# Kernel optimization log

Hardware: AMD Instinct MI355X
Metric: run time of the kernel (lower is better)

## Reference

```python
import jax, jax.numpy as jnp
import numpy as np

NUM_ITER = 3
NUM_SLOTS = 8
SLOT_SIZE = 128
MLP_HIDDEN = 256
EPSILON = 1e-8
INPUT_SIZE = 128
LN_EPS = 1e-5


def layer_norm(x):
    # parameter-free LayerNorm over last dim (LayerNorm() built with no args)
    mu = jnp.mean(x, axis=-1, keepdims=True)
    var = jnp.mean(jnp.square(x - mu), axis=-1, keepdims=True)
    return (x - mu) * jax.lax.rsqrt(var + LN_EPS)


def setup_inputs() -> dict:
    key = jax.random.key(0)
    ks = jax.random.split(key, 16)
    B, N, Din, D, H = 128, 4096, INPUT_SIZE, SLOT_SIZE, MLP_HIDDEN
    s_in = 1.0 / np.sqrt(Din)
    s_d = 1.0 / np.sqrt(D)
    s_h = 1.0 / np.sqrt(H)
    return {
        "inputs": jax.random.normal(ks[0], (B, N, Din), jnp.float32),
        "slots_noise": jax.random.normal(ks[1], (B, NUM_SLOTS, D), jnp.float32),
        "slots_mu": jax.random.normal(ks[2], (1, 1, D), jnp.float32),
        "slots_log_sigma": jax.random.normal(ks[3], (1, 1, D), jnp.float32) * 0.1,
        "Wq": jax.random.normal(ks[4], (D, D), jnp.float32) * s_d,
        "Wk": jax.random.normal(ks[5], (D, Din), jnp.float32) * s_in,
        "Wv": jax.random.normal(ks[6], (D, Din), jnp.float32) * s_in,
        "W_ih": jax.random.normal(ks[7], (3 * D, D), jnp.float32) * s_d,
        "W_hh": jax.random.normal(ks[8], (3 * D, D), jnp.float32) * s_d,
        "b_ih": jax.random.normal(ks[9], (3 * D,), jnp.float32) * s_d,
        "b_hh": jax.random.normal(ks[10], (3 * D,), jnp.float32) * s_d,
        "W1": jax.random.normal(ks[11], (H, D), jnp.float32) * s_d,
        "b1": jnp.zeros((H,), jnp.float32),
        "W2": jax.random.normal(ks[12], (D, H), jnp.float32) * s_h,
        "b2": jnp.zeros((D,), jnp.float32),
    }


def gru_cell(x, h, W_ih, W_hh, b_ih, b_hh):
    # PyTorch GRU, single step. x, h: (..., D)
    gx = x @ W_ih.T + b_ih  # (..., 3D)
    gh = h @ W_hh.T + b_hh
    D = h.shape[-1]
    xr, xz, xn = gx[..., :D], gx[..., D:2 * D], gx[..., 2 * D:]
    hr, hz, hn = gh[..., :D], gh[..., D:2 * D], gh[..., 2 * D:]
    r = jax.nn.sigmoid(xr + hr)
    z = jax.nn.sigmoid(xz + hz)
    n = jnp.tanh(xn + r * hn)
    return (1.0 - z) * n + z * h


def reference(inputs, slots_noise, slots_mu, slots_log_sigma, Wq, Wk, Wv,
              W_ih, W_hh, b_ih, b_hh, W1, b1, W2, b2):
    scale = 1.0 / np.sqrt(SLOT_SIZE)
    x = layer_norm(inputs)                      # (B, N, Din)
    k = x @ Wk.T                                # (B, N, D)
    v = x @ Wv.T                                # (B, N, D)
    slots = slots_mu + jnp.exp(slots_log_sigma) * slots_noise  # (B, S, D)
    for _ in range(NUM_ITER):
        slots_n = layer_norm(slots)             # NOTE: GRU hidden is the NORMED slots (matches source)
        q = slots_n @ Wq.T                      # (B, S, D)
        logits = jnp.einsum("bnd,bsd->bns", k, q) * scale  # (B, N, S)
        attn = jax.nn.softmax(logits, axis=-1) + EPSILON
        attn = attn / jnp.sum(attn, axis=-2, keepdims=True)
        updates = jnp.einsum("bns,bnd->bsd", attn, v)      # (B, S, D)
        slots = gru_cell(updates, slots_n, W_ih, W_hh, b_ih, b_hh)
        slots = slots + (jax.nn.relu(layer_norm(slots) @ W1.T + b1) @ W2.T + b2)
    return slots
```

## Files before the change

### kernel.cpp

```cpp
#include <hip/hip_runtime.h>
#include <math.h>


typedef __attribute__((ext_vector_type(4))) float fx4;
typedef __attribute__((ext_vector_type(8))) short sx8;
typedef __attribute__((ext_vector_type(8))) __bf16 bfx8;
typedef __attribute__((ext_vector_type(4))) unsigned short ux4;

static __device__ __forceinline__ fx4 MFMA(sx8 a, sx8 b, fx4 c) {
  return __builtin_amdgcn_mfma_f32_16x16x32_bf16(
      __builtin_bit_cast(bfx8, a), __builtin_bit_cast(bfx8, b), c, 0, 0, 0);
}

static __device__ __forceinline__ unsigned short f2bf(float f) {
  union { float f; unsigned u; } x; x.f = f;
  unsigned r = x.u + 0x7fffu + ((x.u >> 16) & 1u);
  return (unsigned short)(r >> 16);
}
static __device__ __forceinline__ float bf2f(unsigned short u) {
  union { unsigned u; float f; } x; x.u = ((unsigned)u) << 16; return x.f;
}

__global__ __launch_bounds__(256) void k_fold(
    const float* __restrict__ Wq, const float* __restrict__ Wk,
    const float* __restrict__ Wih, const float* __restrict__ Wv,
    float* __restrict__ Wqk, float* __restrict__ Wihv) {
  int idx = blockIdx.x * 256 + threadIdx.x;
  if (idx < 16384) {
    int e = idx >> 7, c = idx & 127;
    float s = 0.f;
#pragma unroll 4
    for (int d = 0; d < 128; d++) s += Wq[d * 128 + e] * Wk[d * 128 + c];
    Wqk[idx] = s * 0.08838834764831845f;
    return;
  }
  idx -= 16384;
  if (idx < 49152) {
    int g = idx >> 7, c = idx & 127;
    float s = 0.f;
#pragma unroll 4
    for (int d = 0; d < 128; d++) s += Wih[g * 128 + d] * Wv[d * 128 + c];
    Wihv[idx] = s;
  }
}

__global__ __launch_bounds__(256) void k_pack(
    const float* __restrict__ noise, const float* __restrict__ mu,
    const float* __restrict__ lsig, const float* __restrict__ Wqk,
    const float* __restrict__ Wihv, const float* __restrict__ Whh,
    const float* __restrict__ W1, const float* __restrict__ W2,
    float* __restrict__ slots, unsigned short* __restrict__ wqk_b,
    unsigned short* __restrict__ wihv_b, unsigned short* __restrict__ whh_b,
    unsigned short* __restrict__ w1_b, unsigned short* __restrict__ w2_b) {
  int idx = blockIdx.x * 256 + threadIdx.x;
  if (idx < 131072) {
    int d = idx & 127;
    slots[idx] = mu[d] + expf(lsig[d]) * noise[idx];
    return;
  }
  idx -= 131072;
  if (idx < 16384) {
    wqk_b[idx] = f2bf(Wqk[(idx & 127) * 128 + (idx >> 7)]);
    return;
  }
  idx -= 16384;
  if (idx < 49152) { wihv_b[idx] = f2bf(Wihv[idx]); return; }
  idx -= 49152;
  if (idx < 49152) { whh_b[idx] = f2bf(Whh[idx]); return; }
  idx -= 49152;
  if (idx < 32768) { w1_b[idx] = f2bf(W1[idx]); return; }
  idx -= 32768;
  w2_b[idx] = f2bf(W2[idx]);
}

__global__ __launch_bounds__(256) void k_ln(
    const float* __restrict__ x, unsigned short* __restrict__ ln16) {
  long row = (long)blockIdx.x * 8 + (threadIdx.x >> 5);
  int c4 = (threadIdx.x & 31) * 4;
  fx4 t = *(const fx4*)(x + row * 128 + c4);
  float s = t.x + t.y + t.z + t.w;
  float s2 = t.x * t.x + t.y * t.y + t.z * t.z + t.w * t.w;
#pragma unroll
  for (int m = 1; m < 32; m <<= 1) {
    s += __shfl_xor(s, m, 64);
    s2 += __shfl_xor(s2, m, 64);
  }
  float mean = s * 0.0078125f;
  float rstd = rsqrtf(s2 * 0.0078125f - mean * mean + 1e-5f);
  ux4 o;
  o.x = f2bf((t.x - mean) * rstd);
  o.y = f2bf((t.y - mean) * rstd);
  o.z = f2bf((t.z - mean) * rstd);
  o.w = f2bf((t.w - mean) * rstd);
  *(ux4*)(ln16 + row * 128 + c4) = o;
}

__global__ __launch_bounds__(64) void k_slot_pre(
    const float* __restrict__ slots, const unsigned short* __restrict__ wqk_b,
    float* __restrict__ slots_n, unsigned short* __restrict__ q2_b) {
  __shared__ __align__(16) short xf[4 * 64 * 8];
  int l = threadIdx.x;
  int r = l & 15, seg = l >> 4;
  long rowbase = (long)blockIdx.x * 16;
  {
    const float* xp = slots + (rowbase + r) * 128 + seg * 32;
    float* snp = slots_n + (rowbase + r) * 128 + seg * 32;
    float v[32];
    float s = 0.f, s2 = 0.f;
#pragma unroll
    for (int i = 0; i < 8; i++) {
      fx4 t = *(const fx4*)(xp + i * 4);
      v[i * 4 + 0] = t.x; v[i * 4 + 1] = t.y; v[i * 4 + 2] = t.z; v[i * 4 + 3] = t.w;
      s += t.x + t.y + t.z + t.w;
      s2 += t.x * t.x + t.y * t.y + t.z * t.z + t.w * t.w;
    }
    s += __shfl_xor(s, 16, 64);  s += __shfl_xor(s, 32, 64);
    s2 += __shfl_xor(s2, 16, 64); s2 += __shfl_xor(s2, 32, 64);
    float mean = s * 0.0078125f;
    float var = s2 * 0.0078125f - mean * mean;
    float rstd = rsqrtf(var + 1e-5f);
#pragma unroll
    for (int i = 0; i < 8; i++) {
      fx4 t = {(v[i * 4 + 0] - mean) * rstd, (v[i * 4 + 1] - mean) * rstd,
               (v[i * 4 + 2] - mean) * rstd, (v[i * 4 + 3] - mean) * rstd};
      *(fx4*)(snp + i * 4) = t;
      v[i * 4 + 0] = t.x; v[i * 4 + 1] = t.y; v[i * 4 + 2] = t.z; v[i * 4 + 3] = t.w;
    }
#pragma unroll
    for (int q = 0; q < 4; q++) {
      sx8 t;
#pragma unroll
      for (int j = 0; j < 8; j++) t[j] = (short)f2bf(v[q * 8 + j]);
      *(sx8*)&xf[(seg * 64 + (r + 16 * q)) * 8] = t;
    }
  }
  __syncthreads();
  const fx4 z4 = {0.f, 0.f, 0.f, 0.f};
  fx4 acc[8];
#pragma unroll
  for (int nt = 0; nt < 8; nt++) acc[nt] = z4;
#pragma unroll
  for (int ks = 0; ks < 4; ks++) {
    sx8 a = *(const sx8*)&xf[(ks * 64 + l) * 8];
#pragma unroll
    for (int nt = 0; nt < 8; nt++) {
      sx8 bfr = *(const sx8*)(wqk_b + (nt * 16 + (l & 15)) * 128 + ks * 32 + (l >> 4) * 8);
      acc[nt] = MFMA(a, bfr, acc[nt]);
    }
  }
  int cl = l & 15, rq = (l >> 4) * 4;
#pragma unroll
  for (int nt = 0; nt < 8; nt++)
#pragma unroll
    for (int rg = 0; rg < 4; rg++)
      q2_b[(rowbase + rq + rg) * 128 + nt * 16 + cl] = f2bf(acc[nt][rg]);
}

__global__ __launch_bounds__(256) void k_attn(
    const unsigned short* __restrict__ ln16, const unsigned short* __restrict__ q2b,
    float* __restrict__ upd_part, float* __restrict__ sattn_part) {
  __shared__ __align__(16) float abuf[4 * 1024];
  __shared__ float sattnbuf[4 * 8];
  int tid = threadIdx.x, w = tid >> 6, l = tid & 63;
  int b = blockIdx.x >> 4, c = blockIdx.x & 15;
  long base = (long)b * 4096 + (c * 4 + w) * 64;
  const unsigned short* xt = ln16 + base * 128;
  int s = l & 15, qd = (l >> 4) * 8;
  sx8 qf[4];
#pragma unroll
  for (int ks = 0; ks < 4; ks++) {
    if (s < 8) {
      qf[ks] = *(const sx8*)(q2b + ((long)b * 8 + s) * 128 + ks * 32 + qd);
    } else {
      sx8 t;
#pragma unroll
      for (int j = 0; j < 8; j++) t[j] = 0;
      qf[ks] = t;
    }
  }
  sx8 a[4][4];
#pragma unroll
  for (int mt = 0; mt < 4; mt++)
#pragma unroll
    for (int ks = 0; ks < 4; ks++)
      a[mt][ks] = *(const sx8*)(xt + (mt * 16 + s) * 128 + ks * 32 + qd);
  const fx4 z4 = {0.f, 0.f, 0.f, 0.f};
  float sat_loc = 0.f;
  float ua[4][4] = {};
  int d0 = (l & 31) * 4, s0 = (l >> 5) * 4;
  float* attnw = abuf + w * 1024;
#pragma unroll
  for (int mt = 0; mt < 4; mt++) {
    fx4 cc = z4;
#pragma unroll
    for (int ks = 0; ks < 4; ks++) cc = MFMA(a[mt][ks], qf[ks], cc);
#pragma unroll
    for (int rg = 0; rg < 4; rg++) {
      float lg = cc[rg];
      float mx = lg;
      mx = fmaxf(mx, __shfl_xor(mx, 1, 64));
      mx = fmaxf(mx, __shfl_xor(mx, 2, 64));
      mx = fmaxf(mx, __shfl_xor(mx, 4, 64));
      float p = __expf(lg - mx);
      float sm = p;
      sm += __shfl_xor(sm, 1, 64);
      sm += __shfl_xor(sm, 2, 64);
      sm += __shfl_xor(sm, 4, 64);
      float at = p / sm + 1e-8f;
      if (s < 8) sat_loc += at;
      attnw[(mt * 16 + (l >> 4) * 4 + rg) * 16 + s] = at;
    }
  }
#pragma unroll 2
  for (int n0 = 0; n0 < 64; n0 += 8) {
    ux4 vv[8]; fx4 at4[8];
#pragma unroll
    for (int u = 0; u < 8; u++) {
      vv[u] = *(const ux4*)(xt + (n0 + u) * 128 + d0);
      at4[u] = *(const fx4*)&attnw[(n0 + u) * 16 + s0];
    }
#pragma unroll
    for (int u = 0; u < 8; u++) {
      float v0 = bf2f(vv[u].x), v1 = bf2f(vv[u].y), v2 = bf2f(vv[u].z), v3 = bf2f(vv[u].w);
#pragma unroll
      for (int si = 0; si < 4; si++) {
        float av = at4[u][si];
        ua[si][0] += av * v0; ua[si][1] += av * v1;
        ua[si][2] += av * v2; ua[si][3] += av * v3;
      }
    }
  }
#pragma unroll
  for (int si = 0; si < 4; si++) {
    fx4 tv = {ua[si][0], ua[si][1], ua[si][2], ua[si][3]};
    *(fx4*)&attnw[(s0 + si) * 128 + d0] = tv;
  }
  sat_loc += __shfl_xor(sat_loc, 16, 64);
  sat_loc += __shfl_xor(sat_loc, 32, 64);
  if (l < 8) sattnbuf[w * 8 + l] = sat_loc;
  __syncthreads();
  {
    int i = tid * 4;
    fx4 o = *(const fx4*)&abuf[i] + *(const fx4*)&abuf[1024 + i] +
            *(const fx4*)&abuf[2048 + i] + *(const fx4*)&abuf[3072 + i];
    *(fx4*)(upd_part + ((size_t)(b * 16 + c)) * 1024 + i) = o;
    if (tid < 8)
      sattn_part[(b * 16 + c) * 8 + tid] =
          sattnbuf[tid] + sattnbuf[8 + tid] + sattnbuf[16 + tid] + sattnbuf[24 + tid];
  }
}

__global__ __launch_bounds__(256) void k_slot_post(
    const float* __restrict__ upd_part, const float* __restrict__ sattn_part,
    float* __restrict__ slots_n,
    const unsigned short* __restrict__ wihv_b, const unsigned short* __restrict__ whh_b,
    const float* __restrict__ b_ih, const float* __restrict__ b_hh,
    const unsigned short* __restrict__ w1_b, const float* __restrict__ b1,
    const unsigned short* __restrict__ w2_b, const float* __restrict__ b2,
    const unsigned short* __restrict__ wqk_b,
    unsigned short* __restrict__ q2_b, float* __restrict__ out_final, int final_flag) {
  __shared__ __align__(16) char smem[78336];
  float* gx = (float*)smem;
  float* gh = (float*)(smem + 24576);
  float* xred = gx;
  short* xfr = (short*)(smem + 49152);
  short* hfr = (short*)(smem + 53248);
  short* ynf = (short*)(smem + 57344);
  short* y1f = (short*)(smem + 61440);
  float* snew = (float*)(smem + 69632);
  float* satred = (float*)(smem + 78080);
  int tid = threadIdx.x, w = tid >> 6, l = tid & 63;
  int rowbase = blockIdx.x * 16;
  int r = l & 15, seg = l >> 4;
  {
    int row = rowbase + r;
    int bb = row >> 3, ss = row & 7;
    float a[32];
#pragma unroll
    for (int i = 0; i < 32; i++) a[i] = 0.f;
    float satsum = 0.f;
#pragma unroll
    for (int ci = 0; ci < 4; ci++) {
      int ch = bb * 16 + w * 4 + ci;
      const float* up = upd_part + (size_t)ch * 1024 + ss * 128 + seg * 32;
#pragma unroll
      for (int i = 0; i < 8; i++) {
        fx4 t = *(const fx4*)(up + i * 4);
        a[i * 4 + 0] += t.x; a[i * 4 + 1] += t.y; a[i * 4 + 2] += t.z; a[i * 4 + 3] += t.w;
      }
      satsum += sattn_part[ch * 8 + ss];
    }
#pragma unroll
    for (int i = 0; i < 8; i++) {
      fx4 t = {a[i * 4], a[i * 4 + 1], a[i * 4 + 2], a[i * 4 + 3]};
      *(fx4*)&xred[w * 2048 + r * 128 + seg * 32 + i * 4] = t;
    }
    if (seg == 0) satred[w * 16 + r] = satsum;
  }
  __syncthreads();
  if (w == 0) {
    float inv = 1.f / (satred[r] + satred[16 + r] + satred[32 + r] + satred[48 + r]);
    float a[32];
#pragma unroll
    for (int i = 0; i < 8; i++) {
      fx4 t = *(const fx4*)&xred[r * 128 + seg * 32 + i * 4];
      fx4 t1 = *(const fx4*)&xred[2048 + r * 128 + seg * 32 + i * 4];
      fx4 t2 = *(const fx4*)&xred[4096 + r * 128 + seg * 32 + i * 4];
      fx4 t3 = *(const fx4*)&xred[6144 + r * 128 + seg * 32 + i * 4];
      t = t + t1 + t2 + t3;
      a[i * 4 + 0] = t.x * inv; a[i * 4 + 1] = t.y * inv;
      a[i * 4 + 2] = t.z * inv; a[i * 4 + 3] = t.w * inv;
    }
#pragma unroll
    for (int q = 0; q < 4; q++) {
      sx8 t;
#pragma unroll
      for (int j = 0; j < 8; j++) t[j] = (short)f2bf(a[q * 8 + j]);
      *(sx8*)&xfr[(seg * 64 + (r + 16 * q)) * 8] = t;
    }
  } else if (w == 1) {
    const float* hp = slots_n + (long)(rowbase + r) * 128 + seg * 32;
#pragma unroll
    for (int q = 0; q < 4; q++) {
      fx4 t0 = *(const fx4*)(hp + q * 8);
      fx4 t1 = *(const fx4*)(hp + q * 8 + 4);
      sx8 t;
      t[0] = (short)f2bf(t0.x); t[1] = (short)f2bf(t0.y);
      t[2] = (short)f2bf(t0.z); t[3] = (short)f2bf(t0.w);
      t[4] = (short)f2bf(t1.x); t[5] = (short)f2bf(t1.y);
      t[6] = (short)f2bf(t1.z); t[7] = (short)f2bf(t1.w);
      *(sx8*)&hfr[(seg * 64 + (r + 16 * q)) * 8] = t;
    }
  }
  __syncthreads();
  const fx4 z4 = {0.f, 0.f, 0.f, 0.f};
  {
    fx4 ax[6], ah[6];
#pragma unroll
    for (int j = 0; j < 6; j++) { ax[j] = z4; ah[j] = z4; }
#pragma unroll
    for (int ks = 0; ks < 4; ks++) {
      sx8 a_x = *(const sx8*)&xfr[(ks * 64 + l) * 8];
      sx8 a_h = *(const sx8*)&hfr[(ks * 64 + l) * 8];
#pragma unroll
      for (int j = 0; j < 6; j++) {
        int nt = w * 6 + j;
        sx8 bx = *(const sx8*)(wihv_b + (nt * 16 + (l & 15)) * 128 + ks * 32 + (l >> 4) * 8);
        sx8 bh = *(const sx8*)(whh_b + (nt * 16 + (l & 15)) * 128 + ks * 32 + (l >> 4) * 8);
        ax[j] = MFMA(a_x, bx, ax[j]);
        ah[j] = MFMA(a_h, bh, ah[j]);
      }
    }
#pragma unroll
    for (int j = 0; j < 6; j++) {
      int col = (w * 6 + j) * 16 + (l & 15);
#pragma unroll
      for (int rg = 0; rg < 4; rg++) {
        int row = (l >> 4) * 4 + rg;
        gx[row * 384 + col] = ax[j][rg];
        gh[row * 384 + col] = ah[j][rg];
      }
    }
  }
  __syncthreads();
  {
    int row = tid >> 4, j0 = (tid & 15) * 8;
#pragma unroll
    for (int j = j0; j < j0 + 8; j++) {
      float xr = gx[row * 384 + j] + b_ih[j];
      float xz = gx[row * 384 + 128 + j] + b_ih[128 + j];
      float xn = gx[row * 384 + 256 + j] + b_ih[256 + j];
      float hr = gh[row * 384 + j] + b_hh[j];
      float hz = gh[row * 384 + 128 + j] + b_hh[128 + j];
      float hn = gh[row * 384 + 256 + j] + b_hh[256 + j];
      float rr = 1.f / (1.f + __expf(-(xr + hr)));
      float zz = 1.f / (1.f + __expf(-(xz + hz)));
      float nn = tanhf(xn + rr * hn);
      float h = slots_n[(long)(rowbase + row) * 128 + j];
      snew[row * 132 + j] = (1.f - zz) * nn + zz * h;
    }
  }
  __syncthreads();
  if (w == 0) {
    float v[32];
    float s = 0.f, s2 = 0.f;
#pragma unroll
    for (int i = 0; i < 32; i++) {
      float t = snew[r * 132 + seg * 32 + i];
      v[i] = t; s += t; s2 += t * t;
    }
    s += __shfl_xor(s, 16, 64);  s += __shfl_xor(s, 32, 64);
    s2 += __shfl_xor(s2, 16, 64); s2 += __shfl_xor(s2, 32, 64);
    float mean = s * 0.0078125f;
    float var = s2 * 0.0078125f - mean * mean;
    float rstd = rsqrtf(var + 1e-5f);
#pragma unroll
    for (int q = 0; q < 4; q++) {
      sx8 t;
#pragma unroll
      for (int j = 0; j < 8; j++) t[j] = (short)f2bf((v[q * 8 + j] - mean) * rstd);
      *(sx8*)&ynf[(seg * 64 + (r + 16 * q)) * 8] = t;
    }
  }
  __syncthreads();
  {
    fx4 y[4];
#pragma unroll
    for (int j = 0; j < 4; j++) y[j] = z4;
#pragma unroll
    for (int ks = 0; ks < 4; ks++) {
      sx8 a = *(const sx8*)&ynf[(ks * 64 + l) * 8];
#pragma unroll
      for (int j = 0; j < 4; j++) {
        int nt = w * 4 + j;
        sx8 bf = *(const sx8*)(w1_b + (nt * 16 + (l & 15)) * 128 + ks * 32 + (l >> 4) * 8);
        y[j] = MFMA(a, bf, y[j]);
      }
    }
#pragma unroll
    for (int j = 0; j < 4; j++) {
      int col = (w * 4 + j) * 16 + (l & 15);
      float bias = b1[col];
      int ks3 = col >> 5, qq = (col >> 3) & 3, jj = col & 7;
#pragma unroll
      for (int rg = 0; rg < 4; rg++) {
        float val = fmaxf(y[j][rg] + bias, 0.f);
        int m = (l >> 4) * 4 + rg;
        y1f[(ks3 * 64 + m + 16 * qq) * 8 + jj] = (short)f2bf(val);
      }
    }
  }
  __syncthreads();
  {
    fx4 zz2[2];
    zz2[0] = z4; zz2[1] = z4;
#pragma unroll
    for (int ks = 0; ks < 8; ks++) {
      sx8 a = *(const sx8*)&y1f[(ks * 64 + l) * 8];
#pragma unroll
      for (int j = 0; j < 2; j++) {
        sx8 bf = *(const sx8*)(w2_b + ((w * 2 + j) * 16 + (l & 15)) * 256 + ks * 32 + (l >> 4) * 8);
        zz2[j] = MFMA(a, bf, zz2[j]);
      }
    }
#pragma unroll
    for (int j = 0; j < 2; j++) {
      int col = (w * 2 + j) * 16 + (l & 15);
      float bias = b2[col];
#pragma unroll
      for (int rg = 0; rg < 4; rg++) {
        int row = (l >> 4) * 4 + rg;
        snew[row * 132 + col] += zz2[j][rg] + bias;
      }
    }
  }
  __syncthreads();
  if (final_flag) {
    int row = tid >> 4, c8 = (tid & 15) * 8;
    fx4 t0 = *(const fx4*)&snew[row * 132 + c8];
    fx4 t1 = *(const fx4*)&snew[row * 132 + c8 + 4];
    *(fx4*)(out_final + (long)(rowbase + row) * 128 + c8) = t0;
    *(fx4*)(out_final + (long)(rowbase + row) * 128 + c8 + 4) = t1;
    return;
  }
  if (w == 0) {
    float v[32];
    float s = 0.f, s2 = 0.f;
#pragma unroll
    for (int i = 0; i < 32; i++) {
      float t = snew[r * 132 + seg * 32 + i];
      v[i] = t; s += t; s2 += t * t;
    }
    s += __shfl_xor(s, 16, 64);  s += __shfl_xor(s, 32, 64);
    s2 += __shfl_xor(s2, 16, 64); s2 += __shfl_xor(s2, 32, 64);
    float mean = s * 0.0078125f;
    float var = s2 * 0.0078125f - mean * mean;
    float rstd = rsqrtf(var + 1e-5f);
    float* snp = slots_n + (long)(rowbase + r) * 128 + seg * 32;
#pragma unroll
    for (int i = 0; i < 8; i++) {
      fx4 t = {(v[i * 4 + 0] - mean) * rstd, (v[i * 4 + 1] - mean) * rstd,
               (v[i * 4 + 2] - mean) * rstd, (v[i * 4 + 3] - mean) * rstd};
      *(fx4*)(snp + i * 4) = t;
      v[i * 4 + 0] = t.x; v[i * 4 + 1] = t.y; v[i * 4 + 2] = t.z; v[i * 4 + 3] = t.w;
    }
#pragma unroll
    for (int q = 0; q < 4; q++) {
      sx8 t;
#pragma unroll
      for (int j = 0; j < 8; j++) t[j] = (short)f2bf(v[q * 8 + j]);
      *(sx8*)&ynf[(seg * 64 + (r + 16 * q)) * 8] = t;
    }
  }
  __syncthreads();
  {
    fx4 acc2[2];
    acc2[0] = z4; acc2[1] = z4;
#pragma unroll
    for (int ks = 0; ks < 4; ks++) {
      sx8 a = *(const sx8*)&ynf[(ks * 64 + l) * 8];
#pragma unroll
      for (int j = 0; j < 2; j++) {
        int nt = w * 2 + j;
        sx8 bf = *(const sx8*)(wqk_b + (nt * 16 + (l & 15)) * 128 + ks * 32 + (l >> 4) * 8);
        acc2[j] = MFMA(a, bf, acc2[j]);
      }
    }
    int cl = l & 15, rq = (l >> 4) * 4;
#pragma unroll
    for (int j = 0; j < 2; j++) {
      int nt = w * 2 + j;
#pragma unroll
      for (int rg = 0; rg < 4; rg++)
        q2_b[(long)(rowbase + rq + rg) * 128 + nt * 16 + cl] = f2bf(acc2[j][rg]);
    }
  }
}

extern "C" void kernel_launch(void* const* d_in, const int* in_sizes, int n_in,
                              void* d_out, int out_size, void* d_ws, size_t ws_size,
                              hipStream_t stream) {
  (void)in_sizes; (void)n_in; (void)out_size; (void)ws_size;
  const float* x = (const float*)d_in[0];
  const float* noise = (const float*)d_in[1];
  const float* mu = (const float*)d_in[2];
  const float* lsig = (const float*)d_in[3];
  const float* Wq = (const float*)d_in[4];
  const float* Wk = (const float*)d_in[5];
  const float* Wv = (const float*)d_in[6];
  const float* Wih = (const float*)d_in[7];
  const float* Whh = (const float*)d_in[8];
  const float* b_ih = (const float*)d_in[9];
  const float* b_hh = (const float*)d_in[10];
  const float* W1 = (const float*)d_in[11];
  const float* b1 = (const float*)d_in[12];
  const float* W2 = (const float*)d_in[13];
  const float* b2 = (const float*)d_in[14];

  char* ws = (char*)d_ws;
  size_t off = 0;
  auto take = [&](size_t bytes) {
    char* p = ws + off;
    off += (bytes + 255) & ~(size_t)255;
    return p;
  };
  unsigned short* ln16 = (unsigned short*)take(134217728);
  float* Wqk = (float*)take(65536);
  float* Wihv = (float*)take(196608);
  unsigned short* wqk_b = (unsigned short*)take(32768);
  unsigned short* wihv_b = (unsigned short*)take(98304);
  unsigned short* whh_b = (unsigned short*)take(98304);
  unsigned short* w1_b = (unsigned short*)take(65536);
  unsigned short* w2_b = (unsigned short*)take(65536);
  float* slots = (float*)take(524288);
  float* slots_n = (float*)take(524288);
  unsigned short* q2_b = (unsigned short*)take(262144);
  float* upd_part = (float*)take(8388608);
  float* sattn_part = (float*)take(65536);

  k_fold<<<256, 256, 0, stream>>>(Wq, Wk, Wih, Wv, Wqk, Wihv);
  k_pack<<<1216, 256, 0, stream>>>(noise, mu, lsig, Wqk, Wihv, Whh, W1, W2,
                                   slots, wqk_b, wihv_b, whh_b, w1_b, w2_b);
  k_ln<<<65536, 256, 0, stream>>>(x, ln16);
  k_slot_pre<<<64, 64, 0, stream>>>(slots, wqk_b, slots_n, q2_b);
  for (int it = 0; it < 3; it++) {
    k_attn<<<2048, 256, 0, stream>>>(ln16, q2_b, upd_part, sattn_part);
    k_slot_post<<<64, 256, 0, stream>>>(upd_part, sattn_part, slots_n, wihv_b, whh_b,
                                        b_ih, b_hh, w1_b, b1, w2_b, b2, wqk_b,
                                        q2_b, (float*)d_out, (it == 2) ? 1 : 0);
  }
}
```

Baseline: 608.9 us.

## Stage attention tiles in LDS via direct global-to-LDS loads with swizzle

k_attn now uses 128-thread blocks (two waves, 4096 blocks). Each wave loads its 64x128 bf16 token tile once into LDS using global_load_lds with an XOR swizzle, then reads that tile for both the logits MFMA and the attn·v accumulation, instead of fetching it from global memory twice. k_slot_post is relaunched with one batch (8 slots) per block across 128 blocks, reducing twice as many partial chunks and masking the unused rows. The intent is to halve global reads of the large ln16 buffer per iteration and raise parallelism, at the cost of more partial-result traffic and padded MFMA work in slot_post.

```diff
diff --git a/kernel.cpp b/kernel.cpp
--- a/kernel.cpp
+++ b/kernel.cpp
@@ -20,6 +20,9 @@
 static __device__ __forceinline__ float bf2f(unsigned short u) {
   union { unsigned u; float f; } x; x.u = ((unsigned)u) << 16; return x.f;
 }
+
+typedef __attribute__((address_space(1))) const unsigned int gas_uint;
+typedef __attribute__((address_space(3))) unsigned int las_uint;
 
 __global__ __launch_bounds__(256) void k_fold(
     const float* __restrict__ Wq, const float* __restrict__ Wk,
@@ -117,8 +120,7 @@
     s += __shfl_xor(s, 16, 64);  s += __shfl_xor(s, 32, 64);
     s2 += __shfl_xor(s2, 16, 64); s2 += __shfl_xor(s2, 32, 64);
     float mean = s * 0.0078125f;
-    float var = s2 * 0.0078125f - mean * mean;
-    float rstd = rsqrtf(var + 1e-5f);
+    float rstd = rsqrtf(s2 * 0.0078125f - mean * mean + 1e-5f);
 #pragma unroll
     for (int i = 0; i < 8; i++) {
       fx4 t = {(v[i * 4 + 0] - mean) * rstd, (v[i * 4 + 1] - mean) * rstd,
@@ -156,21 +158,29 @@
       q2_b[(rowbase + rq + rg) * 128 + nt * 16 + cl] = f2bf(acc[nt][rg]);
 }
 
-__global__ __launch_bounds__(256) void k_attn(
+__global__ __launch_bounds__(128) void k_attn(
     const unsigned short* __restrict__ ln16, const unsigned short* __restrict__ q2b,
     float* __restrict__ upd_part, float* __restrict__ sattn_part) {
-  __shared__ __align__(16) float abuf[4 * 1024];
-  __shared__ float sattnbuf[4 * 8];
+  __shared__ __align__(16) char smem[40960];
   int tid = threadIdx.x, w = tid >> 6, l = tid & 63;
-  int b = blockIdx.x >> 4, c = blockIdx.x & 15;
-  long base = (long)b * 4096 + (c * 4 + w) * 64;
-  const unsigned short* xt = ln16 + base * 128;
-  int s = l & 15, qd = (l >> 4) * 8;
+  int b = blockIdx.x >> 5, p = blockIdx.x & 31;
+  int tile = p * 2 + w;
+  const unsigned short* tg = ln16 + ((size_t)b * 4096 + tile * 64) * 128;
+  unsigned short* tl = (unsigned short*)(smem + w * 16384);
+  float* attnw = (float*)(smem + 32768 + w * 4096);
+  int hi = l >> 4, s = l & 15;
+#pragma unroll
+  for (int i = 0; i < 16; i++) {
+    int r = i * 4 + hi;
+    int gchunk = r * 16 + (s ^ (r & 15));
+    __builtin_amdgcn_global_load_lds((gas_uint*)(tg + gchunk * 8),
+                                     (las_uint*)(tl + i * 512), 16, 0, 0);
+  }
   sx8 qf[4];
 #pragma unroll
   for (int ks = 0; ks < 4; ks++) {
     if (s < 8) {
-      qf[ks] = *(const sx8*)(q2b + ((long)b * 8 + s) * 128 + ks * 32 + qd);
+      qf[ks] = *(const sx8*)(q2b + ((long)b * 8 + s) * 128 + ks * 32 + hi * 8);
     } else {
       sx8 t;
 #pragma unroll
@@ -178,22 +188,20 @@
       qf[ks] = t;
     }
   }
-  sx8 a[4][4];
-#pragma unroll
-  for (int mt = 0; mt < 4; mt++)
-#pragma unroll
-    for (int ks = 0; ks < 4; ks++)
-      a[mt][ks] = *(const sx8*)(xt + (mt * 16 + s) * 128 + ks * 32 + qd);
+  __builtin_amdgcn_s_waitcnt(0);
+  __syncthreads();
   const fx4 z4 = {0.f, 0.f, 0.f, 0.f};
   float sat_loc = 0.f;
-  float ua[4][4] = {};
-  int d0 = (l & 31) * 4, s0 = (l >> 5) * 4;
-  float* attnw = abuf + w * 1024;
 #pragma unroll
   for (int mt = 0; mt < 4; mt++) {
     fx4 cc = z4;
 #pragma unroll
-    for (int ks = 0; ks < 4; ks++) cc = MFMA(a[mt][ks], qf[ks], cc);
+    for (int ks = 0; ks < 4; ks++) {
+      int r = mt * 16 + s;
+      int slot = r * 16 + ((ks * 4 + hi) ^ s);
+      sx8 a = *(const sx8*)(tl + slot * 8);
+      cc = MFMA(a, qf[ks], cc);
+    }
 #pragma unroll
     for (int rg = 0; rg < 4; rg++) {
       float lg = cc[rg];
@@ -201,23 +209,28 @@
       mx = fmaxf(mx, __shfl_xor(mx, 1, 64));
       mx = fmaxf(mx, __shfl_xor(mx, 2, 64));
       mx = fmaxf(mx, __shfl_xor(mx, 4, 64));
-      float p = __expf(lg - mx);
-      float sm = p;
+      float pp = __expf(lg - mx);
+      float sm = pp;
       sm += __shfl_xor(sm, 1, 64);
       sm += __shfl_xor(sm, 2, 64);
       sm += __shfl_xor(sm, 4, 64);
-      float at = p / sm + 1e-8f;
+      float at = pp / sm + 1e-8f;
       if (s < 8) sat_loc += at;
-      attnw[(mt * 16 + (l >> 4) * 4 + rg) * 16 + s] = at;
-    }
-  }
+      attnw[(mt * 16 + hi * 4 + rg) * 16 + s] = at;
+    }
+  }
+  float ua[4][4] = {};
+  int d0 = (l & 31) * 4, s0 = (l >> 5) * 4;
+  int segp = (l & 31) >> 1, intra = (l & 1) * 4;
 #pragma unroll 2
   for (int n0 = 0; n0 < 64; n0 += 8) {
     ux4 vv[8]; fx4 at4[8];
 #pragma unroll
     for (int u = 0; u < 8; u++) {
-      vv[u] = *(const ux4*)(xt + (n0 + u) * 128 + d0);
-      at4[u] = *(const fx4*)&attnw[(n0 + u) * 16 + s0];
+      int n = n0 + u;
+      int slot = n * 16 + (segp ^ (n & 15));
+      vv[u] = *(const ux4*)(tl + slot * 8 + intra);
+      at4[u] = *(const fx4*)&attnw[n * 16 + s0];
     }
 #pragma unroll
     for (int u = 0; u < 8; u++) {
@@ -237,16 +250,22 @@
   }
   sat_loc += __shfl_xor(sat_loc, 16, 64);
   sat_loc += __shfl_xor(sat_loc, 32, 64);
-  if (l < 8) sattnbuf[w * 8 + l] = sat_loc;
-  __syncthreads();
-  {
-    int i = tid * 4;
-    fx4 o = *(const fx4*)&abuf[i] + *(const fx4*)&abuf[1024 + i] +
-            *(const fx4*)&abuf[2048 + i] + *(const fx4*)&abuf[3072 + i];
-    *(fx4*)(upd_part + ((size_t)(b * 16 + c)) * 1024 + i) = o;
-    if (tid < 8)
-      sattn_part[(b * 16 + c) * 8 + tid] =
-          sattnbuf[tid] + sattnbuf[8 + tid] + sattnbuf[16 + tid] + sattnbuf[24 + tid];
+  if (l < 8) ((float*)tl)[l] = sat_loc;
+  __syncthreads();
+  {
+    int chunk = b * 32 + p;
+    const float* a0 = (const float*)(smem + 32768);
+    const float* a1 = (const float*)(smem + 32768 + 4096);
+    int i = tid * 8;
+    fx4 o0 = *(const fx4*)&a0[i] + *(const fx4*)&a1[i];
+    fx4 o1 = *(const fx4*)&a0[i + 4] + *(const fx4*)&a1[i + 4];
+    *(fx4*)(upd_part + (size_t)chunk * 1024 + i) = o0;
+    *(fx4*)(upd_part + (size_t)chunk * 1024 + i + 4) = o1;
+    if (tid < 8) {
+      const float* s0b = (const float*)smem;
+      const float* s1b = (const float*)(smem + 16384);
+      sattn_part[chunk * 8 + tid] = s0b[tid] + s1b[tid];
+    }
   }
 }
 
@@ -270,46 +289,52 @@
   float* snew = (float*)(smem + 69632);
   float* satred = (float*)(smem + 78080);
   int tid = threadIdx.x, w = tid >> 6, l = tid & 63;
-  int rowbase = blockIdx.x * 16;
+  int bb = blockIdx.x;
+  int rowbase = bb * 8;
   int r = l & 15, seg = l >> 4;
   {
-    int row = rowbase + r;
-    int bb = row >> 3, ss = row & 7;
+    int r8 = l & 7, h8 = l >> 3;
+    float a[16];
+#pragma unroll
+    for (int i = 0; i < 16; i++) a[i] = 0.f;
+    float satsum = 0.f;
+#pragma unroll
+    for (int ci = 0; ci < 8; ci++) {
+      int ch = bb * 32 + w * 8 + ci;
+      const float* up = upd_part + (size_t)ch * 1024 + r8 * 128 + h8 * 16;
+#pragma unroll
+      for (int i = 0; i < 4; i++) {
+        fx4 t = *(const fx4*)(up + i * 4);
+        a[i * 4 + 0] += t.x; a[i * 4 + 1] += t.y;
+        a[i * 4 + 2] += t.z; a[i * 4 + 3] += t.w;
+      }
+      if (h8 == 0) satsum += sattn_part[ch * 8 + r8];
+    }
+#pragma unroll
+    for (int i = 0; i < 4; i++) {
+      fx4 t = {a[i * 4], a[i * 4 + 1], a[i * 4 + 2], a[i * 4 + 3]};
+      *(fx4*)&xred[w * 1024 + r8 * 128 + h8 * 16 + i * 4] = t;
+    }
+    if (h8 == 0) satred[w * 8 + r8] = satsum;
+  }
+  __syncthreads();
+  if (w == 0) {
     float a[32];
-#pragma unroll
-    for (int i = 0; i < 32; i++) a[i] = 0.f;
-    float satsum = 0.f;
-#pragma unroll
-    for (int ci = 0; ci < 4; ci++) {
-      int ch = bb * 16 + w * 4 + ci;
-      const float* up = upd_part + (size_t)ch * 1024 + ss * 128 + seg * 32;
+    if (r < 8) {
+      float inv = 1.f / (satred[r] + satred[8 + r] + satred[16 + r] + satred[24 + r]);
 #pragma unroll
       for (int i = 0; i < 8; i++) {
-        fx4 t = *(const fx4*)(up + i * 4);
-        a[i * 4 + 0] += t.x; a[i * 4 + 1] += t.y; a[i * 4 + 2] += t.z; a[i * 4 + 3] += t.w;
-      }
-      satsum += sattn_part[ch * 8 + ss];
-    }
-#pragma unroll
-    for (int i = 0; i < 8; i++) {
-      fx4 t = {a[i * 4], a[i * 4 + 1], a[i * 4 + 2], a[i * 4 + 3]};
-      *(fx4*)&xred[w * 2048 + r * 128 + seg * 32 + i * 4] = t;
-    }
-    if (seg == 0) satred[w * 16 + r] = satsum;
-  }
-  __syncthreads();
-  if (w == 0) {
-    float inv = 1.f / (satred[r] + satred[16 + r] + satred[32 + r] + satred[48 + r]);
-    float a[32];
-#pragma unroll
-    for (int i = 0; i < 8; i++) {
-      fx4 t = *(const fx4*)&xred[r * 128 + seg * 32 + i * 4];
-      fx4 t1 = *(const fx4*)&xred[2048 + r * 128 + seg * 32 + i * 4];
-      fx4 t2 = *(const fx4*)&xred[4096 + r * 128 + seg * 32 + i * 4];
-      fx4 t3 = *(const fx4*)&xred[6144 + r * 128 + seg * 32 + i * 4];
-      t = t + t1 + t2 + t3;
-      a[i * 4 + 0] = t.x * inv; a[i * 4 + 1] = t.y * inv;
-      a[i * 4 + 2] = t.z * inv; a[i * 4 + 3] = t.w * inv;
+        fx4 t = *(const fx4*)&xred[r * 128 + seg * 32 + i * 4];
+        fx4 t1 = *(const fx4*)&xred[1024 + r * 128 + seg * 32 + i * 4];
+        fx4 t2 = *(const fx4*)&xred[2048 + r * 128 + seg * 32 + i * 4];
+        fx4 t3 = *(const fx4*)&xred[3072 + r * 128 + seg * 32 + i * 4];
+        t = t + t1 + t2 + t3;
+        a[i * 4 + 0] = t.x * inv; a[i * 4 + 1] = t.y * inv;
+        a[i * 4 + 2] = t.z * inv; a[i * 4 + 3] = t.w * inv;
+      }
+    } else {
+#pragma unroll
+      for (int i = 0; i < 32; i++) a[i] = 0.f;
     }
 #pragma unroll
     for (int q = 0; q < 4; q++) {
@@ -319,16 +344,21 @@
       *(sx8*)&xfr[(seg * 64 + (r + 16 * q)) * 8] = t;
     }
   } else if (w == 1) {
-    const float* hp = slots_n + (long)(rowbase + r) * 128 + seg * 32;
 #pragma unroll
     for (int q = 0; q < 4; q++) {
-      fx4 t0 = *(const fx4*)(hp + q * 8);
-      fx4 t1 = *(const fx4*)(hp + q * 8 + 4);
       sx8 t;
-      t[0] = (short)f2bf(t0.x); t[1] = (short)f2bf(t0.y);
-      t[2] = (short)f2bf(t0.z); t[3] = (short)f2bf(t0.w);
-      t[4] = (short)f2bf(t1.x); t[5] = (short)f2bf(t1.y);
-      t[6] = (short)f2bf(t1.z); t[7] = (short)f2bf(t1.w);
+      if (r < 8) {
+        const float* hp = slots_n + (long)(rowbase + r) * 128 + seg * 32;
+        fx4 t0 = *(const fx4*)(hp + q * 8);
+        fx4 t1 = *(const fx4*)(hp + q * 8 + 4);
+        t[0] = (short)f2bf(t0.x); t[1] = (short)f2bf(t0.y);
+        t[2] = (short)f2bf(t0.z); t[3] = (short)f2bf(t0.w);
+        t[4] = (short)f2bf(t1.x); t[5] = (short)f2bf(t1.y);
+        t[6] = (short)f2bf(t1.z); t[7] = (short)f2bf(t1.w);
+      } else {
+#pragma unroll
+        for (int j = 0; j < 8; j++) t[j] = 0;
+      }
       *(sx8*)&hfr[(seg * 64 + (r + 16 * q)) * 8] = t;
     }
   }
@@ -365,19 +395,21 @@
   __syncthreads();
   {
     int row = tid >> 4, j0 = (tid & 15) * 8;
-#pragma unroll
-    for (int j = j0; j < j0 + 8; j++) {
-      float xr = gx[row * 384 + j] + b_ih[j];
-      float xz = gx[row * 384 + 128 + j] + b_ih[128 + j];
-      float xn = gx[row * 384 + 256 + j] + b_ih[256 + j];
-      float hr = gh[row * 384 + j] + b_hh[j];
-      float hz = gh[row * 384 + 128 + j] + b_hh[128 + j];
-      float hn = gh[row * 384 + 256 + j] + b_hh[256 + j];
-      float rr = 1.f / (1.f + __expf(-(xr + hr)));
-      float zz = 1.f / (1.f + __expf(-(xz + hz)));
-      float nn = tanhf(xn + rr * hn);
-      float h = slots_n[(long)(rowbase + row) * 128 + j];
-      snew[row * 132 + j] = (1.f - zz) * nn + zz * h;
+    if (row < 8) {
+#pragma unroll
+      for (int j = j0; j < j0 + 8; j++) {
+        float xr = gx[row * 384 + j] + b_ih[j];
+        float xz = gx[row * 384 + 128 + j] + b_ih[128 + j];
+        float xn = gx[row * 384 + 256 + j] + b_ih[256 + j];
+        float hr = gh[row * 384 + j] + b_hh[j];
+        float hz = gh[row * 384 + 128 + j] + b_hh[128 + j];
+        float hn = gh[row * 384 + 256 + j] + b_hh[256 + j];
+        float rr = 1.f / (1.f + __expf(-(xr + hr)));
+        float zz = 1.f / (1.f + __expf(-(xz + hz)));
+        float nn = tanhf(xn + rr * hn);
+        float h = slots_n[(long)(rowbase + row) * 128 + j];
+        snew[row * 132 + j] = (1.f - zz) * nn + zz * h;
+      }
     }
   }
   __syncthreads();
@@ -386,14 +418,13 @@
     float s = 0.f, s2 = 0.f;
 #pragma unroll
     for (int i = 0; i < 32; i++) {
-      float t = snew[r * 132 + seg * 32 + i];
+      float t = (r < 8) ? snew[r * 132 + seg * 32 + i] : 0.f;
       v[i] = t; s += t; s2 += t * t;
     }
     s += __shfl_xor(s, 16, 64);  s += __shfl_xor(s, 32, 64);
     s2 += __shfl_xor(s2, 16, 64); s2 += __shfl_xor(s2, 32, 64);
     float mean = s * 0.0078125f;
-    float var = s2 * 0.0078125f - mean * mean;
-    float rstd = rsqrtf(var + 1e-5f);
+    float rstd = rsqrtf(s2 * 0.0078125f - mean * mean + 1e-5f);
 #pragma unroll
     for (int q = 0; q < 4; q++) {
       sx8 t;
@@ -457,10 +488,12 @@
   __syncthreads();
   if (final_flag) {
     int row = tid >> 4, c8 = (tid & 15) * 8;
-    fx4 t0 = *(const fx4*)&snew[row * 132 + c8];
-    fx4 t1 = *(const fx4*)&snew[row * 132 + c8 + 4];
-    *(fx4*)(out_final + (long)(rowbase + row) * 128 + c8) = t0;
-    *(fx4*)(out_final + (long)(rowbase + row) * 128 + c8 + 4) = t1;
+    if (row < 8) {
+      fx4 t0 = *(const fx4*)&snew[row * 132 + c8];
+      fx4 t1 = *(const fx4*)&snew[row * 132 + c8 + 4];
+      *(fx4*)(out_final + (long)(rowbase + row) * 128 + c8) = t0;
+      *(fx4*)(out_final + (long)(rowbase + row) * 128 + c8 + 4) = t1;
+    }
     return;
   }
   if (w == 0) {
@@ -468,20 +501,18 @@
     float s = 0.f, s2 = 0.f;
 #pragma unroll
     for (int i = 0; i < 32; i++) {
-      float t = snew[r * 132 + seg * 32 + i];
+      float t = (r < 8) ? snew[r * 132 + seg * 32 + i] : 0.f;
       v[i] = t; s += t; s2 += t * t;
     }
     s += __shfl_xor(s, 16, 64);  s += __shfl_xor(s, 32, 64);
     s2 += __shfl_xor(s2, 16, 64); s2 += __shfl_xor(s2, 32, 64);
     float mean = s * 0.0078125f;
-    float var = s2 * 0.0078125f - mean * mean;
-    float rstd = rsqrtf(var + 1e-5f);
-    float* snp = slots_n + (long)(rowbase + r) * 128 + seg * 32;
+    float rstd = rsqrtf(s2 * 0.0078125f - mean * mean + 1e-5f);
 #pragma unroll
     for (int i = 0; i < 8; i++) {
       fx4 t = {(v[i * 4 + 0] - mean) * rstd, (v[i * 4 + 1] - mean) * rstd,
                (v[i * 4 + 2] - mean) * rstd, (v[i * 4 + 3] - mean) * rstd};
-      *(fx4*)(snp + i * 4) = t;
+      if (r < 8) *(fx4*)(slots_n + (long)(rowbase + r) * 128 + seg * 32 + i * 4) = t;
       v[i * 4 + 0] = t.x; v[i * 4 + 1] = t.y; v[i * 4 + 2] = t.z; v[i * 4 + 3] = t.w;
     }
 #pragma unroll
@@ -507,12 +538,14 @@
       }
     }
     int cl = l & 15, rq = (l >> 4) * 4;
-#pragma unroll
-    for (int j = 0; j < 2; j++) {
-      int nt = w * 2 + j;
-#pragma unroll
-      for (int rg = 0; rg < 4; rg++)
-        q2_b[(long)(rowbase + rq + rg) * 128 + nt * 16 + cl] = f2bf(acc2[j][rg]);
+    if (rq < 8) {
+#pragma unroll
+      for (int j = 0; j < 2; j++) {
+        int nt = w * 2 + j;
+#pragma unroll
+        for (int rg = 0; rg < 4; rg++)
+          q2_b[(long)(rowbase + rq + rg) * 128 + nt * 16 + cl] = f2bf(acc2[j][rg]);
+      }
     }
   }
 }
@@ -555,8 +588,8 @@
   float* slots = (float*)take(524288);
   float* slots_n = (float*)take(524288);
   unsigned short* q2_b = (unsigned short*)take(262144);
-  float* upd_part = (float*)take(8388608);
-  float* sattn_part = (float*)take(65536);
+  float* upd_part = (float*)take(16777216);
+  float* sattn_part = (float*)take(131072);
 
   k_fold<<<256, 256, 0, stream>>>(Wq, Wk, Wih, Wv, Wqk, Wihv);
   k_pack<<<1216, 256, 0, stream>>>(noise, mu, lsig, Wqk, Wihv, Whh, W1, W2,
@@ -564,9 +597,9 @@
   k_ln<<<65536, 256, 0, stream>>>(x, ln16);
   k_slot_pre<<<64, 64, 0, stream>>>(slots, wqk_b, slots_n, q2_b);
   for (int it = 0; it < 3; it++) {
-    k_attn<<<2048, 256, 0, stream>>>(ln16, q2_b, upd_part, sattn_part);
-    k_slot_post<<<64, 256, 0, stream>>>(upd_part, sattn_part, slots_n, wihv_b, whh_b,
-                                        b_ih, b_hh, w1_b, b1, w2_b, b2, wqk_b,
-                                        q2_b, (float*)d_out, (it == 2) ? 1 : 0);
-  }
-}
+    k_attn<<<4096, 128, 0, stream>>>(ln16, q2_b, upd_part, sattn_part);
+    k_slot_post<<<128, 256, 0, stream>>>(upd_part, sattn_part, slots_n, wihv_b, whh_b,
+                                         b_ih, b_hh, w1_b, b1, w2_b, b2, wqk_b,
+                                         q2_b, (float*)d_out, (it == 2) ? 1 : 0);
+  }
+}
```

New measurement: 609.5 us. Within noise of the previous version (+0.1%).
